# Optimization experiments

Hardware: AMD Instinct MI355X
Metric: run time of the kernel (lower is better)

Reference implementation:

```python
import jax, jax.numpy as jnp
import numpy as np

EMBED_DIM = 1024
BATCH, SEQ = 4, 2048


def setup_inputs() -> dict:
    key = jax.random.key(0)
    kx, kq, kk, kv = jax.random.split(key, 4)
    return {
        "x": jax.random.normal(kx, (BATCH, SEQ, EMBED_DIM), dtype=jnp.float32),
        "q_weight": jax.random.normal(kq, (EMBED_DIM, EMBED_DIM), dtype=jnp.float32),
        "k_weight": jax.random.normal(kk, (EMBED_DIM, EMBED_DIM), dtype=jnp.float32),
        "v_weight": jax.random.normal(kv, (EMBED_DIM, EMBED_DIM), dtype=jnp.float32),
    }


def reference(x, q_weight, k_weight, v_weight):
    # x: [b, s, d]
    d = x.shape[-1]
    Q = jnp.einsum('bsd,de->bse', x, q_weight)
    K = jnp.einsum('bsd,de->bse', x, k_weight)
    V = jnp.einsum('bsd,de->bse', x, v_weight)
    scores = jnp.einsum('bqe,bke->bqk', Q, K) / jnp.sqrt(jnp.float32(d))
    attn = jax.nn.softmax(scores, axis=-1)
    out = jnp.einsum('bqk,bke->bqe', attn, V)
    return out
```

## Files before the change

kernel.cpp:

```cpp
#include <hip/hip_runtime.h>
#include <hip/hip_bf16.h>


typedef _Float16 half8 __attribute__((ext_vector_type(8)));
typedef _Float16 half4v __attribute__((ext_vector_type(4)));
typedef float f32x16 __attribute__((ext_vector_type(16)));

#define GLOBAL_AS __attribute__((address_space(1)))
#define LDS_AS __attribute__((address_space(3)))

__device__ __forceinline__ void gll16(const _Float16* g, _Float16* l) {
    __builtin_amdgcn_global_load_lds((GLOBAL_AS const void*)g, (LDS_AS void*)l, 16, 0, 0);
}

template <int NPROD, int OUTMODE>
__global__ __launch_bounds__(256) void gemm_nt(
    const _Float16* __restrict__ A0, const _Float16* __restrict__ A1,
    const _Float16* __restrict__ B0, const _Float16* __restrict__ B1,
    float* __restrict__ Cf, _Float16* __restrict__ C0, _Float16* __restrict__ C1,
    int lda, int ldb, int ldc, int K,
    long sA, long sB, long sC, float scale, float scale2) {
    constexpr int NTILES = (NPROD == 3) ? 4 : 2;
    __shared__ alignas(16) _Float16 smem[NTILES * 4096];
    _Float16* sA0 = smem;
    _Float16* sB0 = smem + 4096;
    _Float16* sA1 = (NPROD == 3) ? smem + 8192 : smem;
    _Float16* sB1 = (NPROD == 3) ? smem + 12288 : smem;

    const int tid = threadIdx.x;
    const int wave = tid >> 6, lane = tid & 63;
    const int wm = (wave >> 1) * 64, wn = (wave & 1) * 64;
    const int q2 = lane >> 5, r32 = lane & 31;

    const long zA = (long)blockIdx.z * sA;
    const long zB = (long)blockIdx.z * sB;
    const long zC = (long)blockIdx.z * sC;

    const float sc = (blockIdx.y * 2 < gridDim.y) ? scale : scale2;

    const int trow = tid >> 2;
    const int tcol = (((tid & 3) - ((tid >> 3) & 3) - ((tid >> 6) & 3)) & 3) * 8;
    const _Float16* gA0 = A0 + zA + (long)(blockIdx.x * 128 + trow) * lda + tcol;
    const _Float16* gB0 = B0 + zB + (long)(blockIdx.y * 128 + trow) * ldb + tcol;
    const _Float16* gA1 = (NPROD == 3) ? (A1 + zA + (long)(blockIdx.x * 128 + trow) * lda + tcol) : nullptr;
    const _Float16* gB1 = (NPROD == 3) ? (B1 + zB + (long)(blockIdx.y * 128 + trow) * ldb + tcol) : nullptr;

    f32x16 acc[2][2];
#pragma unroll
    for (int i = 0; i < 2; ++i)
#pragma unroll
        for (int j = 0; j < 2; ++j)
#pragma unroll
            for (int r = 0; r < 16; ++r) acc[i][j][r] = 0.f;

    const int ldsoff = tid * 8;
    const int fbase = q2 + (r32 >> 1) + (r32 >> 4);

    for (int k0 = 0; k0 < K; k0 += 32) {
        __syncthreads();
        gll16(gA0, sA0 + ldsoff);
        gll16(gA0 + 64 * lda, sA0 + ldsoff + 2048);
        gll16(gB0, sB0 + ldsoff);
        gll16(gB0 + 64 * ldb, sB0 + ldsoff + 2048);
        if (NPROD == 3) {
            gll16(gA1, sA1 + ldsoff);
            gll16(gA1 + 64 * lda, sA1 + ldsoff + 2048);
            gll16(gB1, sB1 + ldsoff);
            gll16(gB1 + 64 * ldb, sB1 + ldsoff + 2048);
        }
        gA0 += 32; gB0 += 32;
        if (NPROD == 3) { gA1 += 32; gB1 += 32; }
        __syncthreads();

        half8 a0[2][2], b0[2][2], a1[2][2], b1[2][2];
#pragma unroll
        for (int i = 0; i < 2; ++i)
#pragma unroll
            for (int h = 0; h < 2; ++h) {
                const int pp = ((fbase + 2 * i + 2 * h) & 3) * 8;
                a0[i][h] = *(const half8*)(sA0 + (wm + i * 32 + r32) * 32 + pp);
                b0[i][h] = *(const half8*)(sB0 + (wn + i * 32 + r32) * 32 + pp);
                if (NPROD == 3) {
                    a1[i][h] = *(const half8*)(sA1 + (wm + i * 32 + r32) * 32 + pp);
                    b1[i][h] = *(const half8*)(sB1 + (wn + i * 32 + r32) * 32 + pp);
                }
            }
#pragma unroll
        for (int i = 0; i < 2; ++i)
#pragma unroll
            for (int j = 0; j < 2; ++j)
#pragma unroll
                for (int h = 0; h < 2; ++h) {
                    acc[i][j] = __builtin_amdgcn_mfma_f32_32x32x16_f16(a0[i][h], b0[j][h], acc[i][j], 0, 0, 0);
                    if (NPROD == 3) {
                        acc[i][j] = __builtin_amdgcn_mfma_f32_32x32x16_f16(a0[i][h], b1[j][h], acc[i][j], 0, 0, 0);
                        acc[i][j] = __builtin_amdgcn_mfma_f32_32x32x16_f16(a1[i][h], b0[j][h], acc[i][j], 0, 0, 0);
                    }
                }
    }

    const int crow0 = blockIdx.x * 128 + wm + 4 * q2;
    const int ccol0 = blockIdx.y * 128 + wn + r32;
#pragma unroll
    for (int i = 0; i < 2; ++i)
#pragma unroll
        for (int j = 0; j < 2; ++j)
#pragma unroll
            for (int r = 0; r < 16; ++r) {
                int row = crow0 + i * 32 + (r & 3) + 8 * (r >> 2);
                long off = zC + (long)row * ldc + (ccol0 + j * 32);
                float v = acc[i][j][r] * sc;
                if (OUTMODE == 0) {
                    Cf[off] = v;
                } else if (OUTMODE == 2) {
                    C0[off] = (_Float16)v;
                } else {
                    _Float16 h = (_Float16)v;
                    C0[off] = h;
                    C1[off] = (_Float16)(v - (float)h);
                }
            }
}

__global__ __launch_bounds__(256) void prep_fused(
    const float* __restrict__ x, _Float16* __restrict__ x0, _Float16* __restrict__ x1,
    long n4, int nsplit,
    const float* __restrict__ wq, const float* __restrict__ wk,
    const float* __restrict__ wv,
    _Float16* __restrict__ qk0, _Float16* __restrict__ qk1,
    _Float16* __restrict__ v0, _Float16* __restrict__ v1) {
    __shared__ float t[32][33];
    if ((int)blockIdx.x < nsplit) {
        long i = (long)blockIdx.x * 256 + threadIdx.x;
        if (i >= n4) return;
        float4 v = ((const float4*)x)[i];
        float a[4] = {v.x, v.y, v.z, v.w};
        half4v h, l;
#pragma unroll
        for (int c = 0; c < 4; ++c) {
            h[c] = (_Float16)a[c];
            l[c] = (_Float16)(a[c] - (float)h[c]);
        }
        ((half4v*)x0)[i] = h;
        ((half4v*)x1)[i] = l;
        return;
    }
    const int idx = blockIdx.x - nsplit;
    const int z = idx >> 10;
    const int tile = idx & 1023;
    const float* in = (z == 0) ? wq : (z == 1) ? wk : wv;
    _Float16* o0 = (z == 0) ? qk0 : (z == 1) ? qk0 + 1024 * 1024 : v0;
    _Float16* o1 = (z == 0) ? qk1 : (z == 1) ? qk1 + 1024 * 1024 : v1;

    const int c0 = (tile & 31) * 32, r0 = (tile >> 5) * 32;
    const int tx = threadIdx.x & 31, ty = threadIdx.x >> 5;
#pragma unroll
    for (int i = 0; i < 32; i += 8)
        t[ty + i][tx] = in[(long)(r0 + ty + i) * 1024 + c0 + tx];
    __syncthreads();
#pragma unroll
    for (int i = 0; i < 32; i += 8) {
        float v = t[tx][ty + i];
        _Float16 h = (_Float16)v;
        long o = (long)(c0 + ty + i) * 1024 + r0 + tx;
        o0[o] = h;
        o1[o] = (_Float16)(v - (float)h);
    }
}

__global__ __launch_bounds__(256) void softmax_rows(const float* __restrict__ S,
                                                    _Float16* __restrict__ P) {
    const int n = 2048;
    const long base = (long)blockIdx.x * n;
    const float4* row4 = (const float4*)(S + base);
    const int tid = threadIdx.x;
    const int wave = tid >> 6;

    float4 v0 = row4[tid * 2];
    float4 v1 = row4[tid * 2 + 1];
    float v[8] = {v0.x, v0.y, v0.z, v0.w, v1.x, v1.y, v1.z, v1.w};
    float lm = -3.4e38f;
#pragma unroll
    for (int t = 0; t < 8; ++t) lm = fmaxf(lm, v[t]);
#pragma unroll
    for (int o = 32; o > 0; o >>= 1) lm = fmaxf(lm, __shfl_xor(lm, o));
    __shared__ float redm[4];
    __shared__ float reds[4];
    if ((tid & 63) == 0) redm[wave] = lm;
    __syncthreads();
    lm = fmaxf(fmaxf(redm[0], redm[1]), fmaxf(redm[2], redm[3]));

    float e[8];
    float ls = 0.f;
#pragma unroll
    for (int t = 0; t < 8; ++t) {
        e[t] = __expf(v[t] - lm);
        ls += e[t];
    }
#pragma unroll
    for (int o = 32; o > 0; o >>= 1) ls += __shfl_xor(ls, o);
    if ((tid & 63) == 0) reds[wave] = ls;
    __syncthreads();
    ls = reds[0] + reds[1] + reds[2] + reds[3];
    const float inv = 1.f / ls;
    half8 p;
#pragma unroll
    for (int t = 0; t < 8; ++t) p[t] = (_Float16)(e[t] * inv);
    ((half8*)(P + base))[tid] = p;
}

extern "C" void kernel_launch(void* const* d_in, const int* in_sizes, int n_in,
                              void* d_out, int out_size, void* d_ws, size_t ws_size,
                              hipStream_t stream) {
    (void)in_sizes; (void)n_in; (void)out_size; (void)ws_size;
    const float* x = (const float*)d_in[0];
    const float* wq = (const float*)d_in[1];
    const float* wk = (const float*)d_in[2];
    const float* wv = (const float*)d_in[3];
    float* out = (float*)d_out;
    char* ws = (char*)d_ws;

    const long MB = 1l << 20;
    _Float16* Wqk0 = (_Float16*)(ws + 0 * MB);
    _Float16* Wqk1 = (_Float16*)(ws + 4 * MB);
    _Float16* Wv0  = (_Float16*)(ws + 8 * MB);
    _Float16* Wv1  = (_Float16*)(ws + 10 * MB);
    _Float16* x0   = (_Float16*)(ws + 12 * MB);
    _Float16* x1   = (_Float16*)(ws + 28 * MB);
    _Float16* P    = (_Float16*)(ws + 12 * MB);
    _Float16* QK0  = (_Float16*)(ws + 44 * MB);
    _Float16* QK1  = (_Float16*)(ws + 76 * MB);
    _Float16* Vt   = (_Float16*)(ws + 108 * MB);
    float*    S    = (float*)(ws + 124 * MB);

    const int B = 4, SEQ = 2048, D = 1024;
    const long M = (long)B * SEQ;
    const long ssq = (long)SEQ * SEQ;
    const int nsplit = (int)((M * D / 4 + 255) / 256);

    prep_fused<<<dim3(nsplit + 3072), dim3(256), 0, stream>>>(
        x, x0, x1, M * D / 4, nsplit, wq, wk, wv, Wqk0, Wqk1, Wv0, Wv1);

    gemm_nt<3, 1><<<dim3(64, 16, 1), dim3(256), 0, stream>>>(
        x0, x1, Wqk0, Wqk1, nullptr, QK0, QK1, D, D, 2 * D, D,
        0, 0, 0, 0.03125f, 1.0f);

    gemm_nt<1, 2><<<dim3(8, 64, 1), dim3(256), 0, stream>>>(
        Wv0, nullptr, x0, nullptr, nullptr, Vt, nullptr, D, D, (int)M, D,
        0, 0, 0, 1.0f, 1.0f);

    gemm_nt<3, 0><<<dim3(16, 16, B), dim3(256), 0, stream>>>(
        QK0, QK1, QK0 + D, QK1 + D, S, nullptr, nullptr, 2 * D, 2 * D, SEQ, D,
        (long)SEQ * 2 * D, (long)SEQ * 2 * D, ssq, 1.0f, 1.0f);

    softmax_rows<<<dim3(B * SEQ), dim3(256), 0, stream>>>(S, P);

    gemm_nt<1, 0><<<dim3(16, 8, B), dim3(256), 0, stream>>>(
        P, nullptr, Vt, nullptr, out, nullptr, nullptr, SEQ, (int)M, D, SEQ,
        ssq, (long)SEQ, (long)SEQ * D, 1.0f, 1.0f);
}
```

Baseline: 421.8 us.

## Register-prefetch next K tile instead of direct global-to-LDS loads

Replaces the global_load_lds direct copies with a software pipeline that loads the next K-slice into registers while the MFMAs for the current slice run, then writes them to LDS at the top of the next iteration. It also reorders the fragment loads per half-K step so fewer fragments are live at once. The aim is to hide global memory latency behind compute, since before each iteration waited for its own loads. The cost is extra VGPRs for the staging registers (up to 8 float4s for the split-precision variant), which may lower occupancy, plus extra VALU/LDS store instructions.

```diff
diff --git a/kernel.cpp b/kernel.cpp
--- a/kernel.cpp
+++ b/kernel.cpp
@@ -5,13 +5,6 @@
 typedef _Float16 half8 __attribute__((ext_vector_type(8)));
 typedef _Float16 half4v __attribute__((ext_vector_type(4)));
 typedef float f32x16 __attribute__((ext_vector_type(16)));
-
-#define GLOBAL_AS __attribute__((address_space(1)))
-#define LDS_AS __attribute__((address_space(3)))
-
-__device__ __forceinline__ void gll16(const _Float16* g, _Float16* l) {
-    __builtin_amdgcn_global_load_lds((GLOBAL_AS const void*)g, (LDS_AS void*)l, 16, 0, 0);
-}
 
 template <int NPROD, int OUTMODE>
 __global__ __launch_bounds__(256) void gemm_nt(
@@ -21,6 +14,7 @@
     int lda, int ldb, int ldc, int K,
     long sA, long sB, long sC, float scale, float scale2) {
     constexpr int NTILES = (NPROD == 3) ? 4 : 2;
+    constexpr int NST = (NPROD == 3) ? 8 : 4;
     __shared__ alignas(16) _Float16 smem[NTILES * 4096];
     _Float16* sA0 = smem;
     _Float16* sB0 = smem + 4096;
@@ -56,47 +50,73 @@
     const int ldsoff = tid * 8;
     const int fbase = q2 + (r32 >> 1) + (r32 >> 4);
 
+    float4 st[NST];
+    {
+        st[0] = *(const float4*)gA0;
+        st[1] = *(const float4*)(gA0 + 64 * lda);
+        st[2] = *(const float4*)gB0;
+        st[3] = *(const float4*)(gB0 + 64 * ldb);
+        if (NPROD == 3) {
+            st[4] = *(const float4*)gA1;
+            st[5] = *(const float4*)(gA1 + 64 * lda);
+            st[6] = *(const float4*)gB1;
+            st[7] = *(const float4*)(gB1 + 64 * ldb);
+        }
+    }
+
     for (int k0 = 0; k0 < K; k0 += 32) {
         __syncthreads();
-        gll16(gA0, sA0 + ldsoff);
-        gll16(gA0 + 64 * lda, sA0 + ldsoff + 2048);
-        gll16(gB0, sB0 + ldsoff);
-        gll16(gB0 + 64 * ldb, sB0 + ldsoff + 2048);
+        *(float4*)(sA0 + ldsoff) = st[0];
+        *(float4*)(sA0 + ldsoff + 2048) = st[1];
+        *(float4*)(sB0 + ldsoff) = st[2];
+        *(float4*)(sB0 + ldsoff + 2048) = st[3];
         if (NPROD == 3) {
-            gll16(gA1, sA1 + ldsoff);
-            gll16(gA1 + 64 * lda, sA1 + ldsoff + 2048);
-            gll16(gB1, sB1 + ldsoff);
-            gll16(gB1 + 64 * ldb, sB1 + ldsoff + 2048);
-        }
+            *(float4*)(sA1 + ldsoff) = st[4];
+            *(float4*)(sA1 + ldsoff + 2048) = st[5];
+            *(float4*)(sB1 + ldsoff) = st[6];
+            *(float4*)(sB1 + ldsoff + 2048) = st[7];
+        }
+        __syncthreads();
+
         gA0 += 32; gB0 += 32;
         if (NPROD == 3) { gA1 += 32; gB1 += 32; }
-        __syncthreads();
-
-        half8 a0[2][2], b0[2][2], a1[2][2], b1[2][2];
-#pragma unroll
-        for (int i = 0; i < 2; ++i)
-#pragma unroll
-            for (int h = 0; h < 2; ++h) {
+        if (k0 + 32 < K) {
+            st[0] = *(const float4*)gA0;
+            st[1] = *(const float4*)(gA0 + 64 * lda);
+            st[2] = *(const float4*)gB0;
+            st[3] = *(const float4*)(gB0 + 64 * ldb);
+            if (NPROD == 3) {
+                st[4] = *(const float4*)gA1;
+                st[5] = *(const float4*)(gA1 + 64 * lda);
+                st[6] = *(const float4*)gB1;
+                st[7] = *(const float4*)(gB1 + 64 * ldb);
+            }
+        }
+
+#pragma unroll
+        for (int h = 0; h < 2; ++h) {
+            half8 a0[2], b0[2], a1[2], b1[2];
+#pragma unroll
+            for (int i = 0; i < 2; ++i) {
                 const int pp = ((fbase + 2 * i + 2 * h) & 3) * 8;
-                a0[i][h] = *(const half8*)(sA0 + (wm + i * 32 + r32) * 32 + pp);
-                b0[i][h] = *(const half8*)(sB0 + (wn + i * 32 + r32) * 32 + pp);
+                a0[i] = *(const half8*)(sA0 + (wm + i * 32 + r32) * 32 + pp);
+                b0[i] = *(const half8*)(sB0 + (wn + i * 32 + r32) * 32 + pp);
                 if (NPROD == 3) {
-                    a1[i][h] = *(const half8*)(sA1 + (wm + i * 32 + r32) * 32 + pp);
-                    b1[i][h] = *(const half8*)(sB1 + (wn + i * 32 + r32) * 32 + pp);
+                    a1[i] = *(const half8*)(sA1 + (wm + i * 32 + r32) * 32 + pp);
+                    b1[i] = *(const half8*)(sB1 + (wn + i * 32 + r32) * 32 + pp);
                 }
             }
 #pragma unroll
-        for (int i = 0; i < 2; ++i)
-#pragma unroll
-            for (int j = 0; j < 2; ++j)
-#pragma unroll
-                for (int h = 0; h < 2; ++h) {
-                    acc[i][j] = __builtin_amdgcn_mfma_f32_32x32x16_f16(a0[i][h], b0[j][h], acc[i][j], 0, 0, 0);
+            for (int i = 0; i < 2; ++i)
+#pragma unroll
+                for (int j = 0; j < 2; ++j) {
+                    acc[i][j] = __builtin_amdgcn_mfma_f32_32x32x16_f16(a0[i], b0[j], acc[i][j], 0, 0, 0);
                     if (NPROD == 3) {
-                        acc[i][j] = __builtin_amdgcn_mfma_f32_32x32x16_f16(a0[i][h], b1[j][h], acc[i][j], 0, 0, 0);
-                        acc[i][j] = __builtin_amdgcn_mfma_f32_32x32x16_f16(a1[i][h], b0[j][h], acc[i][j], 0, 0, 0);
+                        acc[i][j] = __builtin_amdgcn_mfma_f32_32x32x16_f16(a0[i], b1[j], acc[i][j], 0, 0, 0);
+                        acc[i][j] = __builtin_amdgcn_mfma_f32_32x32x16_f16(a1[i], b0[j], acc[i][j], 0, 0, 0);
                     }
                 }
+        }
     }
 
     const int crow0 = blockIdx.x * 128 + wm + 4 * q2;
```

Result: slower. 999.1 us (+136.9%).
